# Performance work log

Hardware: AMD Instinct MI355X
Metric: run time of the kernel (lower is better)

Reference implementation:

```python
import jax, jax.numpy as jnp
import numpy as np
import math

B = 2; T = 512; ND = 256; NDAYS = 24; STRIDE = 4; KLEN = 14
DM = ND * KLEN          # 3584, d_model after unfolding
NLAYERS = 2; DSTATE = 16; DCONV = 4; EXPAND = 2
DI = EXPAND * DM        # 7168 d_inner
DTR = math.ceil(DM / 16)  # 224 dt_rank
NCLS = 41
LOUT = (T - KLEN) // STRIDE + 1  # 125


def setup_inputs():
    key = jax.random.key(0)
    ks = jax.random.split(key, 12)
    f32 = jnp.float32
    neuralInput = jax.random.normal(ks[0], (B, T, ND), f32)
    dayIdx = jax.random.randint(ks[1], (B,), 0, NDAYS)
    # day-specific linear init: identity weight, zero bias (as in BaseDecoder)
    day_w = jnp.tile(jnp.eye(ND, dtype=f32)[None], (NDAYS, 1, 1))
    day_b = jnp.zeros((NDAYS, 1, ND), f32)
    norm_w = jnp.ones((NLAYERS, DM), f32)
    norm_b = jnp.zeros((NLAYERS, DM), f32)
    in_proj_w = 0.02 * jax.random.normal(ks[2], (NLAYERS, 2 * DI, DM), f32)
    conv_w = 0.2 * jax.random.normal(ks[3], (NLAYERS, DI, DCONV), f32)  # depthwise
    conv_b = jnp.zeros((NLAYERS, DI), f32)
    x_proj_w = 0.02 * jax.random.normal(ks[4], (NLAYERS, DTR + 2 * DSTATE, DI), f32)
    s = DTR ** -0.5
    dt_proj_w = jax.random.uniform(ks[5], (NLAYERS, DI, DTR), f32, -s, s)
    # dt bias init: inverse-softplus of dt ~ LogUniform[1e-3, 1e-1]
    dt = jnp.exp(jax.random.uniform(ks[6], (NLAYERS, DI), f32) * (math.log(0.1) - math.log(0.001)) + math.log(0.001))
    dt = jnp.clip(dt, 1e-4, None)
    dt_proj_b = dt + jnp.log(-jnp.expm1(-dt))
    A_log = jnp.broadcast_to(jnp.log(jnp.arange(1, DSTATE + 1, dtype=f32)), (NLAYERS, DI, DSTATE)).copy()
    D_param = jnp.ones((NLAYERS, DI), f32)
    out_proj_w = 0.02 * jax.random.normal(ks[7], (NLAYERS, DM, DI), f32)
    normf_w = jnp.ones((DM,), f32)
    normf_b = jnp.zeros((DM,), f32)
    fc_w = 0.02 * jax.random.normal(ks[8], (NCLS, DM), f32)
    fc_b = jnp.zeros((NCLS,), f32)
    return dict(neuralInput=neuralInput, day_w=day_w, day_b=day_b, norm_w=norm_w, norm_b=norm_b,
                in_proj_w=in_proj_w, conv_w=conv_w, conv_b=conv_b, x_proj_w=x_proj_w,
                dt_proj_w=dt_proj_w, dt_proj_b=dt_proj_b, A_log=A_log, D_param=D_param,
                out_proj_w=out_proj_w, normf_w=normf_w, normf_b=normf_b, fc_w=fc_w, fc_b=fc_b,
                dayIdx=dayIdx)


def _layernorm(x, w, b):
    mu = x.mean(-1, keepdims=True)
    v = jnp.var(x, -1, keepdims=True)
    return (x - mu) * jax.lax.rsqrt(v + 1e-5) * w + b


def _mamba(h, ipw, cw, cb, xpw, dtw, dtb, Alog, Dp, opw):
    # h: (B, L, DM) -> (B, L, DM); unidirectional Mamba, use_fast_path=False math
    Bb, L, _ = h.shape
    xz = h @ ipw.T                              # (B, L, 2*DI)
    x, z = xz[..., :DI], xz[..., DI:]
    # depthwise causal conv1d, kernel DCONV, left pad DCONV-1, truncated to L
    xp = jnp.pad(x, ((0, 0), (DCONV - 1, 0), (0, 0)))
    xc = cb + sum(xp[:, j:j + L, :] * cw[:, j] for j in range(DCONV))
    x = jax.nn.silu(xc)
    x_dbl = x @ xpw.T                           # (B, L, DTR + 2*N)
    dt = x_dbl[..., :DTR]
    Bc = x_dbl[..., DTR:DTR + DSTATE]
    Cc = x_dbl[..., DTR + DSTATE:]
    delta = jax.nn.softplus(dt @ dtw.T + dtb)   # (B, L, DI), delta_softplus=True
    A = -jnp.exp(Alog)                          # (DI, N)
    dA = jnp.exp(delta[..., None] * A)          # (B, L, DI, N)
    dBu = (delta * x)[..., None] * Bc[:, :, None, :]  # (B, L, DI, N)

    def step(hst, inp):
        a, bu, c = inp
        hst = a * hst + bu                      # (B, DI, N)
        return hst, jnp.einsum('bdn,bn->bd', hst, c)

    h0 = jnp.zeros((Bb, DI, DSTATE), h.dtype)
    _, ys = jax.lax.scan(step, h0, (dA.transpose(1, 0, 2, 3), dBu.transpose(1, 0, 2, 3), Cc.transpose(1, 0, 2)))
    y = ys.transpose(1, 0, 2) + x * Dp          # skip term D*u
    y = y * jax.nn.silu(z)                      # gated output
    return y @ opw.T


def reference(neuralInput, day_w, day_b, norm_w, norm_b, in_proj_w, conv_w, conv_b, x_proj_w,
              dt_proj_w, dt_proj_b, A_log, D_param, out_proj_w, normf_w, normf_b, fc_w, fc_b, dayIdx):
    # --- BaseDecoder.forward_preprocessing (gaussianSmoothWidth = 0) ---
    t = jnp.einsum('btd,bdk->btk', neuralInput, day_w[dayIdx]) + day_b[dayIdx]
    t = t / (1.0 + jnp.abs(t))                  # Softsign
    idx = jnp.arange(LOUT)[:, None] * STRIDE + jnp.arange(KLEN)[None, :]
    win = t[:, idx, :]                          # (B, LOUT, KLEN, ND)
    # torch Unfold feature ordering: channel-major then kernel position -> d*KLEN + j
    h = win.transpose(0, 1, 3, 2).reshape(t.shape[0], LOUT, DM)
    # --- stacked Mamba blocks (pre-norm residual) ---
    residual = None
    for i in range(NLAYERS):
        residual = h if residual is None else h + residual
        hn = _layernorm(residual, norm_w[i], norm_b[i])
        h = _mamba(hn, in_proj_w[i], conv_w[i], conv_b[i], x_proj_w[i], dt_proj_w[i],
                   dt_proj_b[i], A_log[i], D_param[i], out_proj_w[i])
    residual = h + residual
    hn = _layernorm(residual, normf_w, normf_b)
    return hn @ fc_w.T + fc_b                   # (B, LOUT, NCLS)
```

## Files before the change

### kernel.cpp

```cpp
#include <hip/hip_runtime.h>
#include <hip/hip_bf16.h>
#include <math.h>

#define BATCH   2
#define TSEQ    512
#define NDIM    256
#define STRIDE_ 4
#define KLEN    14
#define DM      3584
#define DI      7168
#define DTR     224
#define DSTATE  16
#define NCLS    41
#define LOUT    125
#define LPAD    128
#define MROWS   256

typedef __attribute__((ext_vector_type(8))) short bf8_t;
typedef __attribute__((ext_vector_type(4))) float f4_t;

__device__ inline unsigned bfpair(float a, float b) {
    unsigned ua = __builtin_bit_cast(unsigned, a);
    unsigned ub = __builtin_bit_cast(unsigned, b);
    ua = (ua + 0x7fffu + ((ua >> 16) & 1u)) >> 16;
    ub = (ub + 0x7fffu + ((ub >> 16) & 1u)) >> 16;
    return ua | (ub << 16);
}
__device__ inline uint4 pack8(float4 a, float4 b) {
    return make_uint4(bfpair(a.x, a.y), bfpair(a.z, a.w),
                      bfpair(b.x, b.y), bfpair(b.z, b.w));
}

__global__ void day_proj(const float* __restrict__ nI, const float* __restrict__ dw,
                         const float* __restrict__ db, const int* __restrict__ dayIdx,
                         float* __restrict__ t_full) {
    int bi = blockIdx.x;
    int b = bi >> 9;
    int di = dayIdx[b];
    int tid = threadIdx.x;
    __shared__ float a_sh[256];
    a_sh[tid] = nI[(size_t)bi * 256 + tid];
    __syncthreads();
    const float* w = dw + (size_t)di * 65536;
    float acc = db[(size_t)di * 256 + tid];
    #pragma unroll 8
    for (int d = 0; d < 256; ++d) acc = fmaf(a_sh[d], w[d * 256 + tid], acc);
    t_full[(size_t)bi * 256 + tid] = acc / (1.f + fabsf(acc));
}

__global__ void window_k(const float* __restrict__ t_full, float* __restrict__ res) {
    int bl = blockIdx.x;
    int b = bl >> 7, l = bl & 127;
    size_t m = (size_t)b * LPAD + l;
    if (l >= LOUT) {
        for (int c = threadIdx.x; c < DM; c += 256) res[m * DM + c] = 0.f;
        return;
    }
    for (int c = threadIdx.x; c < DM; c += 256) {
        int d = c / KLEN, j = c - d * KLEN;
        res[m * DM + c] = t_full[((size_t)b * TSEQ + l * STRIDE_ + j) * 256 + d];
    }
}

__global__ void ln_pack(const float* __restrict__ res, const float* __restrict__ w,
                        const float* __restrict__ b, short* __restrict__ hnp) {
    int m = blockIdx.x, tid = threadIdx.x;
    const float* row = res + (size_t)m * DM;
    float s = 0.f, ss = 0.f;
    for (int c = tid; c < DM; c += 256) { float v = row[c]; s += v; ss += v * v; }
    #pragma unroll
    for (int o = 32; o; o >>= 1) { s += __shfl_xor(s, o); ss += __shfl_xor(ss, o); }
    __shared__ float sm[8];
    int wid = tid >> 6;
    if ((tid & 63) == 0) { sm[wid] = s; sm[4 + wid] = ss; }
    __syncthreads();
    s = sm[0] + sm[1] + sm[2] + sm[3];
    ss = sm[4] + sm[5] + sm[6] + sm[7];
    float mu = s * (1.f / DM);
    float var = ss * (1.f / DM) - mu * mu;
    float rs = rsqrtf(var + 1e-5f);
    for (int G = tid; G < DM / 8; G += 256) {
        float4 f0 = *(const float4*)(row + G * 8);
        float4 f1 = *(const float4*)(row + G * 8 + 4);
        float4 w0 = *(const float4*)(w + G * 8);
        float4 w1 = *(const float4*)(w + G * 8 + 4);
        float4 b0 = *(const float4*)(b + G * 8);
        float4 b1 = *(const float4*)(b + G * 8 + 4);
        f0.x = (f0.x - mu) * rs * w0.x + b0.x; f0.y = (f0.y - mu) * rs * w0.y + b0.y;
        f0.z = (f0.z - mu) * rs * w0.z + b0.z; f0.w = (f0.w - mu) * rs * w0.w + b0.w;
        f1.x = (f1.x - mu) * rs * w1.x + b1.x; f1.y = (f1.y - mu) * rs * w1.y + b1.y;
        f1.z = (f1.z - mu) * rs * w1.z + b1.z; f1.w = (f1.w - mu) * rs * w1.w + b1.w;
        *(uint4*)&hnp[((size_t)G * 256 + m) * 8] = pack8(f0, f1);
    }
}

__global__ void pack_rows(const float* __restrict__ src, int lda, int nG,
                          short* __restrict__ dst) {
    int m = blockIdx.x;
    const float* row = src + (size_t)m * lda;
    for (int G = threadIdx.x; G < nG; G += 256) {
        float4 f0 = *(const float4*)(row + G * 8);
        float4 f1 = *(const float4*)(row + G * 8 + 4);
        *(uint4*)&dst[((size_t)G * 256 + m) * 8] = pack8(f0, f1);
    }
}

__global__ void zero_k(float* __restrict__ p) {
    size_t i = (size_t)(blockIdx.x * 256 + threadIdx.x) * 4;
    *(float4*)(p + i) = make_float4(0.f, 0.f, 0.f, 0.f);
}

template <int EPI, int NT>
__global__ __launch_bounds__(256)
void gemm_mfma(const short* __restrict__ Ap, const float* __restrict__ W, int ldw,
               float* __restrict__ C, int ldc, int kSteps,
               const float* __restrict__ bias) {
    constexpr int NC = NT / 16;
    __shared__ __align__(16) short a_sh[2][4][2056];
    __shared__ __align__(16) short w_sh[2][4][NT * 8 + 8];
    const int tid = threadIdx.x;
    const int wz = tid >> 6, lane = tid & 63;
    const int g = lane >> 4, i16 = lane & 15;
    const int n0 = blockIdx.x * NT;
    const int sBeg = blockIdx.z * kSteps, sEnd = sBeg + kSteps;
    const int wr = tid >> 3;
    const int wq = tid & 7;

    f4_t acc[4][NC];
    #pragma unroll
    for (int r = 0; r < 4; ++r)
        #pragma unroll
        for (int c = 0; c < NC; ++c) acc[r][c] = (f4_t){0.f, 0.f, 0.f, 0.f};

    const short* arow = Ap + (size_t)tid * 8;
    const float* wbase  = W + (size_t)(n0 + wr) * ldw + wq * 4;
    const float* wbase2 = wbase + (size_t)32 * ldw;

    float4 wv0 = *(const float4*)(wbase + (size_t)sBeg * 32);
    float4 wv1;
    if constexpr (NT == 64) wv1 = *(const float4*)(wbase2 + (size_t)sBeg * 32);
    #pragma unroll
    for (int it = 0; it < 4; ++it)
        __builtin_amdgcn_global_load_lds(
            (const __attribute__((address_space(1))) unsigned int*)(arow + (size_t)(sBeg * 4 + it) * 2048),
            (__attribute__((address_space(3))) unsigned int*)&a_sh[0][it][tid * 8], 16, 0, 0);
    {
        uint2 p0 = {bfpair(wv0.x, wv0.y), bfpair(wv0.z, wv0.w)};
        *(uint2*)&w_sh[0][wq >> 1][wr * 8 + (wq & 1) * 4] = p0;
        if constexpr (NT == 64) {
            uint2 p1 = {bfpair(wv1.x, wv1.y), bfpair(wv1.z, wv1.w)};
            *(uint2*)&w_sh[0][wq >> 1][(wr + 32) * 8 + (wq & 1) * 4] = p1;
        }
    }
    int s1 = (sBeg + 1 < sEnd) ? sBeg + 1 : sEnd - 1;
    wv0 = *(const float4*)(wbase + (size_t)s1 * 32);
    if constexpr (NT == 64) wv1 = *(const float4*)(wbase2 + (size_t)s1 * 32);

    for (int s = sBeg; s < sEnd; ++s) {
        const int cur = (s - sBeg) & 1, nxt = cur ^ 1;
        __syncthreads();
        if (s + 1 < sEnd) {
            #pragma unroll
            for (int it = 0; it < 4; ++it)
                __builtin_amdgcn_global_load_lds(
                    (const __attribute__((address_space(1))) unsigned int*)(arow + (size_t)((s + 1) * 4 + it) * 2048),
                    (__attribute__((address_space(3))) unsigned int*)&a_sh[nxt][it][tid * 8], 16, 0, 0);
            uint2 p0 = {bfpair(wv0.x, wv0.y), bfpair(wv0.z, wv0.w)};
            *(uint2*)&w_sh[nxt][wq >> 1][wr * 8 + (wq & 1) * 4] = p0;
            if constexpr (NT == 64) {
                uint2 p1 = {bfpair(wv1.x, wv1.y), bfpair(wv1.z, wv1.w)};
                *(uint2*)&w_sh[nxt][wq >> 1][(wr + 32) * 8 + (wq & 1) * 4] = p1;
            }
            int s2 = (s + 2 < sEnd) ? s + 2 : sEnd - 1;
            wv0 = *(const float4*)(wbase + (size_t)s2 * 32);
            if constexpr (NT == 64) wv1 = *(const float4*)(wbase2 + (size_t)s2 * 32);
        }
        bf8_t af[4], wf[NC];
        #pragma unroll
        for (int r = 0; r < 4; ++r)
            af[r] = *(const bf8_t*)&a_sh[cur][g][(wz * 64 + r * 16 + i16) * 8];
        #pragma unroll
        for (int c = 0; c < NC; ++c)
            wf[c] = *(const bf8_t*)&w_sh[cur][g][(c * 16 + i16) * 8];
        #pragma unroll
        for (int r = 0; r < 4; ++r)
            #pragma unroll
            for (int c = 0; c < NC; ++c)
                acc[r][c] = __builtin_amdgcn_mfma_f32_16x16x32_bf16(af[r], wf[c], acc[r][c], 0, 0, 0);
    }

    float bv[NC];
    if (EPI == 1) {
        #pragma unroll
        for (int c = 0; c < NC; ++c) bv[c] = bias[n0 + c * 16 + i16];
    }
    #pragma unroll
    for (int r = 0; r < 4; ++r) {
        #pragma unroll
        for (int c = 0; c < NC; ++c) {
            int n = n0 + c * 16 + i16;
            #pragma unroll
            for (int v = 0; v < 4; ++v) {
                int m = wz * 64 + r * 16 + g * 4 + v;
                float val = acc[r][c][v];
                if (EPI == 0) {
                    C[(size_t)m * ldc + n] = val;
                } else if (EPI == 1) {
                    val += bv[c];
                    C[(size_t)m * ldc + n] = (val > 20.f) ? val : log1pf(expf(val));
                } else {
                    atomicAdd(&C[(size_t)m * ldc + n], val);
                }
            }
        }
    }
}

__global__ void conv_silu_pack(const float* __restrict__ xz, const float* __restrict__ cw,
                               const float* __restrict__ cb, float* __restrict__ xq,
                               short* __restrict__ xqp) {
    int bl = blockIdx.x;
    int b = bl / 125, l = bl % 125;
    size_t m = (size_t)b * LPAD + l;
    for (int c0 = threadIdx.x * 8; c0 < DI; c0 += 2048) {
        float v[8];
        float4 cb0 = *(const float4*)(cb + c0);
        float4 cb1 = *(const float4*)(cb + c0 + 4);
        v[0] = cb0.x; v[1] = cb0.y; v[2] = cb0.z; v[3] = cb0.w;
        v[4] = cb1.x; v[5] = cb1.y; v[6] = cb1.z; v[7] = cb1.w;
        #pragma unroll
        for (int j = 0; j < 4; ++j) {
            int lj = l - 3 + j;
            if (lj < 0) continue;
            const float* xr = xz + ((size_t)b * LPAD + lj) * (2 * DI) + c0;
            float4 x0 = *(const float4*)xr;
            float4 x1 = *(const float4*)(xr + 4);
            float xa[8] = {x0.x, x0.y, x0.z, x0.w, x1.x, x1.y, x1.z, x1.w};
            #pragma unroll
            for (int k = 0; k < 8; ++k)
                v[k] = fmaf(xa[k], cw[(c0 + k) * 4 + j], v[k]);
        }
        float4 o0, o1;
        #pragma unroll
        for (int k = 0; k < 8; ++k) {
            float sv = v[k] / (1.f + expf(-v[k]));
            if (k < 4) (&o0.x)[k] = sv; else (&o1.x)[k - 4] = sv;
        }
        *(float4*)(xq + m * DI + c0) = o0;
        *(float4*)(xq + m * DI + c0 + 4) = o1;
        *(uint4*)&xqp[(((size_t)c0 / 8) * 256 + m) * 8] = pack8(o0, o1);
    }
}

__global__ void scan_kernel(const float* __restrict__ delta, const float* __restrict__ xq,
                            const float* __restrict__ xdbl, const float* __restrict__ xz,
                            const float* __restrict__ Alog, const float* __restrict__ Dp,
                            float* __restrict__ y) {
    int tid = threadIdx.x;
    int sg = tid & 3;
    int c = blockIdx.x * 64 + (tid >> 2);
    int b = blockIdx.y;
    float As[4], st[4];
    #pragma unroll
    for (int k = 0; k < 4; ++k) {
        As[k] = -expf(Alog[(size_t)c * DSTATE + sg * 4 + k]);
        st[k] = 0.f;
    }
    float dp = Dp[c];
    size_t mb = (size_t)b * LPAD;
    float d_c = delta[mb * DI + c];
    float x_c = xq[mb * DI + c];
    float z_c = xz[mb * (2 * DI) + DI + c];
    float4 B_c = *(const float4*)(xdbl + mb * 256 + DTR + sg * 4);
    float4 C_c = *(const float4*)(xdbl + mb * 256 + DTR + DSTATE + sg * 4);
    for (int l = 0; l < LOUT; ++l) {
        float d_n = d_c, x_n = x_c, z_n = z_c;
        float4 B_n = B_c, C_n = C_c;
        if (l + 1 < LOUT) {
            size_t m = mb + l + 1;
            d_n = delta[m * DI + c];
            x_n = xq[m * DI + c];
            z_n = xz[m * (2 * DI) + DI + c];
            B_n = *(const float4*)(xdbl + m * 256 + DTR + sg * 4);
            C_n = *(const float4*)(xdbl + m * 256 + DTR + DSTATE + sg * 4);
        }
        float du = d_c * x_c;
        float yv = 0.f;
        #pragma unroll
        for (int k = 0; k < 4; ++k) {
            st[k] = fmaf(expf(d_c * As[k]), st[k], du * (&B_c.x)[k]);
            yv = fmaf(st[k], (&C_c.x)[k], yv);
        }
        yv += __shfl_xor(yv, 1);
        yv += __shfl_xor(yv, 2);
        if (sg == 0)
            y[(mb + l) * DI + c] = (yv + x_c * dp) * (z_c / (1.f + expf(-z_c)));
        d_c = d_n; x_c = x_n; z_c = z_n; B_c = B_n; C_c = C_n;
    }
}

__global__ void ln_fc(const float* __restrict__ res, const float* __restrict__ wf,
                      const float* __restrict__ bf, const float* __restrict__ fcw,
                      const float* __restrict__ fcb, float* __restrict__ out) {
    __shared__ __align__(16) float hs[DM];
    __shared__ float sm[8];
    int bl = blockIdx.x;
    int b = bl / 125, l = bl % 125;
    size_t m = (size_t)b * LPAD + l;
    int tid = threadIdx.x;
    const float* row = res + m * DM;
    float s = 0.f, ss = 0.f;
    for (int c = tid; c < DM; c += 256) { float v = row[c]; s += v; ss += v * v; }
    #pragma unroll
    for (int o = 32; o; o >>= 1) { s += __shfl_xor(s, o); ss += __shfl_xor(ss, o); }
    int wid = tid >> 6;
    if ((tid & 63) == 0) { sm[wid] = s; sm[4 + wid] = ss; }
    __syncthreads();
    s = sm[0] + sm[1] + sm[2] + sm[3];
    ss = sm[4] + sm[5] + sm[6] + sm[7];
    float mu = s * (1.f / DM);
    float var = ss * (1.f / DM) - mu * mu;
    float rs = rsqrtf(var + 1e-5f);
    for (int c = tid; c < DM; c += 256) hs[c] = (row[c] - mu) * rs * wf[c] + bf[c];
    __syncthreads();
    int lane = tid & 63;
    for (int n = wid; n < NCLS; n += 4) {
        const float* wrow = fcw + (size_t)n * DM;
        float a0 = 0.f, a1 = 0.f, a2 = 0.f, a3 = 0.f;
        for (int k = lane; k < DM; k += 256) {
            a0 = fmaf(hs[k],       wrow[k],       a0);
            a1 = fmaf(hs[k + 64],  wrow[k + 64],  a1);
            a2 = fmaf(hs[k + 128], wrow[k + 128], a2);
            a3 = fmaf(hs[k + 192], wrow[k + 192], a3);
        }
        float acc = (a0 + a1) + (a2 + a3);
        #pragma unroll
        for (int o = 32; o; o >>= 1) acc += __shfl_xor(acc, o);
        if (lane == 0) out[((size_t)b * LOUT + l) * NCLS + n] = acc + fcb[n];
    }
}

extern "C" void kernel_launch(void* const* d_in, const int* in_sizes, int n_in,
                              void* d_out, int out_size, void* d_ws, size_t ws_size,
                              hipStream_t stream) {
    (void)in_sizes; (void)n_in; (void)out_size; (void)ws_size;
    const float* nI   = (const float*)d_in[0];
    const float* dw   = (const float*)d_in[1];
    const float* db   = (const float*)d_in[2];
    const float* nw   = (const float*)d_in[3];
    const float* nb   = (const float*)d_in[4];
    const float* ipw  = (const float*)d_in[5];
    const float* cw   = (const float*)d_in[6];
    const float* cb   = (const float*)d_in[7];
    const float* xpw  = (const float*)d_in[8];
    const float* dtw  = (const float*)d_in[9];
    const float* dtb  = (const float*)d_in[10];
    const float* Alog = (const float*)d_in[11];
    const float* Dp   = (const float*)d_in[12];
    const float* opw  = (const float*)d_in[13];
    const float* nfw  = (const float*)d_in[14];
    const float* nfb  = (const float*)d_in[15];
    const float* fcw  = (const float*)d_in[16];
    const float* fcb  = (const float*)d_in[17];
    const int*   dayI = (const int*)d_in[18];
    float* out = (float*)d_out;

    float* wsf = (float*)d_ws;
    float* t_full = wsf; wsf += 262144;
    float* res    = wsf; wsf += (size_t)MROWS * DM;
    float* xz     = wsf; wsf += (size_t)MROWS * 2 * DI;
    float* xq     = wsf; wsf += (size_t)MROWS * DI;
    float* xdbl   = wsf; wsf += (size_t)MROWS * 256;
    float* delta  = wsf; wsf += (size_t)MROWS * DI;
    float* yb     = wsf; wsf += (size_t)MROWS * DI;
    short* wss = (short*)wsf;
    short* hnp   = wss; wss += (size_t)MROWS * DM;
    short* xqp   = wss; wss += (size_t)MROWS * DI;
    short* xdblp = wss; wss += (size_t)MROWS * DTR;
    short* ybp   = wss; wss += (size_t)MROWS * DI;

    day_proj<<<dim3(BATCH * TSEQ), 256, 0, stream>>>(nI, dw, db, dayI, t_full);
    window_k<<<dim3(MROWS), 256, 0, stream>>>(t_full, res);

    for (int i = 0; i < 2; ++i) {
        ln_pack<<<dim3(MROWS), 256, 0, stream>>>(res, nw + (size_t)i * DM, nb + (size_t)i * DM, hnp);
        gemm_mfma<0, 32><<<dim3(448, 1, 1), 256, 0, stream>>>(
            hnp, ipw + (size_t)i * 2 * DI * DM, DM, xz, 2 * DI, 112, nullptr);
        conv_silu_pack<<<dim3(BATCH * LOUT), 256, 0, stream>>>(
            xz, cw + (size_t)i * DI * 4, cb + (size_t)i * DI, xq, xqp);
        zero_k<<<dim3(64), 256, 0, stream>>>(xdbl);
        gemm_mfma<2, 32><<<dim3(8, 1, 28), 256, 0, stream>>>(
            xqp, xpw + (size_t)i * 256 * DI, DI, xdbl, 256, 8, nullptr);
        pack_rows<<<dim3(MROWS), 256, 0, stream>>>(xdbl, 256, DTR / 8, xdblp);
        gemm_mfma<1, 32><<<dim3(224, 1, 1), 256, 0, stream>>>(
            xdblp, dtw + (size_t)i * DI * DTR, DTR, delta, DI, 7, dtb + (size_t)i * DI);
        scan_kernel<<<dim3(DI / 64, BATCH), 256, 0, stream>>>(
            delta, xq, xdbl, xz, Alog + (size_t)i * DI * DSTATE, Dp + (size_t)i * DI, yb);
        pack_rows<<<dim3(MROWS), 256, 0, stream>>>(yb, DI, DI / 8, ybp);
        gemm_mfma<2, 32><<<dim3(112, 1, 4), 256, 0, stream>>>(
            ybp, opw + (size_t)i * DM * DI, DI, res, DM, 56, nullptr);
    }

    ln_fc<<<dim3(BATCH * LOUT), 256, 0, stream>>>(res, nfw, nfb, fcw, fcb, out);
}
```

Baseline: 1.381 ms.

## Triple-buffer GEMM loads and replace atomic split-K with partial buffers plus fused reduces

The bf16 MFMA GEMM moves from double to triple buffering in LDS. It uses explicit vmcnt waits and one barrier per k-step, so global-to-LDS copies run two steps ahead of compute. Split-K GEMMs no longer atomically add into a zeroed output. Each split instead writes its own partial slice, and the slices are summed in a new reduce_pack_bc kernel, inside ln_pack (residual add) and inside ln_fc. The zero and pack_rows kernels go away: the scan writes the packed bf16 y layout directly, and the reduce kernel packs xdbl. The cost is extra workspace and partial-sum traffic, plus scattered 2-byte stores from the scan.

```diff
diff --git a/kernel.cpp b/kernel.cpp
--- a/kernel.cpp
+++ b/kernel.cpp
@@ -62,15 +62,28 @@
     }
 }
 
-__global__ void ln_pack(const float* __restrict__ res, const float* __restrict__ w,
-                        const float* __restrict__ b, short* __restrict__ hnp) {
+template <bool ADD>
+__global__ void ln_pack(float* __restrict__ res, const float* __restrict__ part,
+                        const float* __restrict__ w, const float* __restrict__ b,
+                        short* __restrict__ hnp) {
+    __shared__ __align__(16) float hs[DM];
+    __shared__ float sm[8];
     int m = blockIdx.x, tid = threadIdx.x;
-    const float* row = res + (size_t)m * DM;
+    float* row = res + (size_t)m * DM;
     float s = 0.f, ss = 0.f;
-    for (int c = tid; c < DM; c += 256) { float v = row[c]; s += v; ss += v * v; }
+    for (int c = tid; c < DM; c += 256) {
+        float v = row[c];
+        if (ADD) {
+            v += part[((size_t)0 * MROWS + m) * DM + c]
+               + part[((size_t)1 * MROWS + m) * DM + c]
+               + part[((size_t)2 * MROWS + m) * DM + c]
+               + part[((size_t)3 * MROWS + m) * DM + c];
+            row[c] = v;
+        }
+        hs[c] = v; s += v; ss += v * v;
+    }
     #pragma unroll
     for (int o = 32; o; o >>= 1) { s += __shfl_xor(s, o); ss += __shfl_xor(ss, o); }
-    __shared__ float sm[8];
     int wid = tid >> 6;
     if ((tid & 63) == 0) { sm[wid] = s; sm[4 + wid] = ss; }
     __syncthreads();
@@ -80,8 +93,8 @@
     float var = ss * (1.f / DM) - mu * mu;
     float rs = rsqrtf(var + 1e-5f);
     for (int G = tid; G < DM / 8; G += 256) {
-        float4 f0 = *(const float4*)(row + G * 8);
-        float4 f1 = *(const float4*)(row + G * 8 + 4);
+        float4 f0 = *(const float4*)(hs + G * 8);
+        float4 f1 = *(const float4*)(hs + G * 8 + 4);
         float4 w0 = *(const float4*)(w + G * 8);
         float4 w1 = *(const float4*)(w + G * 8 + 4);
         float4 b0 = *(const float4*)(b + G * 8);
@@ -94,30 +107,14 @@
     }
 }
 
-__global__ void pack_rows(const float* __restrict__ src, int lda, int nG,
-                          short* __restrict__ dst) {
-    int m = blockIdx.x;
-    const float* row = src + (size_t)m * lda;
-    for (int G = threadIdx.x; G < nG; G += 256) {
-        float4 f0 = *(const float4*)(row + G * 8);
-        float4 f1 = *(const float4*)(row + G * 8 + 4);
-        *(uint4*)&dst[((size_t)G * 256 + m) * 8] = pack8(f0, f1);
-    }
-}
-
-__global__ void zero_k(float* __restrict__ p) {
-    size_t i = (size_t)(blockIdx.x * 256 + threadIdx.x) * 4;
-    *(float4*)(p + i) = make_float4(0.f, 0.f, 0.f, 0.f);
-}
-
 template <int EPI, int NT>
 __global__ __launch_bounds__(256)
 void gemm_mfma(const short* __restrict__ Ap, const float* __restrict__ W, int ldw,
-               float* __restrict__ C, int ldc, int kSteps,
+               float* __restrict__ C, int ldc, int kSteps, size_t cStrideZ,
                const float* __restrict__ bias) {
     constexpr int NC = NT / 16;
-    __shared__ __align__(16) short a_sh[2][4][2056];
-    __shared__ __align__(16) short w_sh[2][4][NT * 8 + 8];
+    __shared__ __align__(16) short a_sh[3][4][2056];
+    __shared__ __align__(16) short w_sh[3][4][NT * 8 + 8];
     const int tid = threadIdx.x;
     const int wz = tid >> 6, lane = tid & 63;
     const int g = lane >> 4, i16 = lane & 15;
@@ -125,6 +122,7 @@
     const int sBeg = blockIdx.z * kSteps, sEnd = sBeg + kSteps;
     const int wr = tid >> 3;
     const int wq = tid & 7;
+    C += (size_t)blockIdx.z * cStrideZ;
 
     f4_t acc[4][NC];
     #pragma unroll
@@ -133,47 +131,34 @@
         for (int c = 0; c < NC; ++c) acc[r][c] = (f4_t){0.f, 0.f, 0.f, 0.f};
 
     const short* arow = Ap + (size_t)tid * 8;
-    const float* wbase  = W + (size_t)(n0 + wr) * ldw + wq * 4;
-    const float* wbase2 = wbase + (size_t)32 * ldw;
-
+    const float* wbase = W + (size_t)(n0 + wr) * ldw + wq * 4;
+
+    auto stageA = [&](int s, int buf) {
+        #pragma unroll
+        for (int it = 0; it < 4; ++it)
+            __builtin_amdgcn_global_load_lds(
+                (const __attribute__((address_space(1))) unsigned int*)(arow + (size_t)(s * 4 + it) * 2048),
+                (__attribute__((address_space(3))) unsigned int*)&a_sh[buf][it][tid * 8], 16, 0, 0);
+    };
+
+    stageA(sBeg, 0);
     float4 wv0 = *(const float4*)(wbase + (size_t)sBeg * 32);
-    float4 wv1;
-    if constexpr (NT == 64) wv1 = *(const float4*)(wbase2 + (size_t)sBeg * 32);
-    #pragma unroll
-    for (int it = 0; it < 4; ++it)
-        __builtin_amdgcn_global_load_lds(
-            (const __attribute__((address_space(1))) unsigned int*)(arow + (size_t)(sBeg * 4 + it) * 2048),
-            (__attribute__((address_space(3))) unsigned int*)&a_sh[0][it][tid * 8], 16, 0, 0);
+    stageA(sBeg + 1, 1);
+    float4 wv1 = *(const float4*)(wbase + (size_t)(sBeg + 1) * 32);
     {
         uint2 p0 = {bfpair(wv0.x, wv0.y), bfpair(wv0.z, wv0.w)};
         *(uint2*)&w_sh[0][wq >> 1][wr * 8 + (wq & 1) * 4] = p0;
-        if constexpr (NT == 64) {
-            uint2 p1 = {bfpair(wv1.x, wv1.y), bfpair(wv1.z, wv1.w)};
-            *(uint2*)&w_sh[0][wq >> 1][(wr + 32) * 8 + (wq & 1) * 4] = p1;
-        }
-    }
-    int s1 = (sBeg + 1 < sEnd) ? sBeg + 1 : sEnd - 1;
-    wv0 = *(const float4*)(wbase + (size_t)s1 * 32);
-    if constexpr (NT == 64) wv1 = *(const float4*)(wbase2 + (size_t)s1 * 32);
-
-    for (int s = sBeg; s < sEnd; ++s) {
-        const int cur = (s - sBeg) & 1, nxt = cur ^ 1;
-        __syncthreads();
-        if (s + 1 < sEnd) {
-            #pragma unroll
-            for (int it = 0; it < 4; ++it)
-                __builtin_amdgcn_global_load_lds(
-                    (const __attribute__((address_space(1))) unsigned int*)(arow + (size_t)((s + 1) * 4 + it) * 2048),
-                    (__attribute__((address_space(3))) unsigned int*)&a_sh[nxt][it][tid * 8], 16, 0, 0);
-            uint2 p0 = {bfpair(wv0.x, wv0.y), bfpair(wv0.z, wv0.w)};
-            *(uint2*)&w_sh[nxt][wq >> 1][wr * 8 + (wq & 1) * 4] = p0;
-            if constexpr (NT == 64) {
-                uint2 p1 = {bfpair(wv1.x, wv1.y), bfpair(wv1.z, wv1.w)};
-                *(uint2*)&w_sh[nxt][wq >> 1][(wr + 32) * 8 + (wq & 1) * 4] = p1;
-            }
-            int s2 = (s + 2 < sEnd) ? s + 2 : sEnd - 1;
-            wv0 = *(const float4*)(wbase + (size_t)s2 * 32);
-            if constexpr (NT == 64) wv1 = *(const float4*)(wbase2 + (size_t)s2 * 32);
+    }
+    asm volatile("s_waitcnt vmcnt(5) lgkmcnt(0)" ::: "memory");
+    __builtin_amdgcn_s_barrier();
+
+    float4 wv2;
+    for (int t = sBeg; t < sEnd; ++t) {
+        const int cur = (t - sBeg) % 3;
+        const bool has2 = (t + 2 < sEnd);
+        if (has2) {
+            stageA(t + 2, (cur + 2) % 3);
+            wv2 = *(const float4*)(wbase + (size_t)(t + 2) * 32);
         }
         bf8_t af[4], wf[NC];
         #pragma unroll
@@ -187,6 +172,17 @@
             #pragma unroll
             for (int c = 0; c < NC; ++c)
                 acc[r][c] = __builtin_amdgcn_mfma_f32_16x16x32_bf16(af[r], wf[c], acc[r][c], 0, 0, 0);
+        if (t + 1 < sEnd) {
+            uint2 p1 = {bfpair(wv1.x, wv1.y), bfpair(wv1.z, wv1.w)};
+            *(uint2*)&w_sh[(cur + 1) % 3][wq >> 1][wr * 8 + (wq & 1) * 4] = p1;
+            if (has2) {
+                wv1 = wv2;
+                asm volatile("s_waitcnt vmcnt(5) lgkmcnt(0)" ::: "memory");
+            } else {
+                asm volatile("s_waitcnt vmcnt(0) lgkmcnt(0)" ::: "memory");
+            }
+            __builtin_amdgcn_s_barrier();
+        }
     }
 
     float bv[NC];
@@ -205,14 +201,29 @@
                 float val = acc[r][c][v];
                 if (EPI == 0) {
                     C[(size_t)m * ldc + n] = val;
-                } else if (EPI == 1) {
+                } else {
                     val += bv[c];
                     C[(size_t)m * ldc + n] = (val > 20.f) ? val : log1pf(expf(val));
-                } else {
-                    atomicAdd(&C[(size_t)m * ldc + n], val);
                 }
             }
         }
+    }
+}
+
+__global__ void reduce_pack_bc(const float* __restrict__ part, float* __restrict__ xdbl,
+                               short* __restrict__ xdblp) {
+    int m = blockIdx.x, tid = threadIdx.x;
+    float v = 0.f;
+    #pragma unroll 4
+    for (int z = 0; z < 28; ++z) v += part[((size_t)z * MROWS + m) * 256 + tid];
+    xdbl[(size_t)m * 256 + tid] = v;
+    __shared__ float buf[256];
+    buf[tid] = v;
+    __syncthreads();
+    if (tid < DTR / 8) {
+        float4 f0 = *(const float4*)&buf[tid * 8];
+        float4 f1 = *(const float4*)&buf[tid * 8 + 4];
+        *(uint4*)&xdblp[((size_t)tid * 256 + m) * 8] = pack8(f0, f1);
     }
 }
 
@@ -255,7 +266,7 @@
 __global__ void scan_kernel(const float* __restrict__ delta, const float* __restrict__ xq,
                             const float* __restrict__ xdbl, const float* __restrict__ xz,
                             const float* __restrict__ Alog, const float* __restrict__ Dp,
-                            float* __restrict__ y) {
+                            float* __restrict__ y, short* __restrict__ ybp) {
     int tid = threadIdx.x;
     int sg = tid & 3;
     int c = blockIdx.x * 64 + (tid >> 2);
@@ -293,15 +304,21 @@
         }
         yv += __shfl_xor(yv, 1);
         yv += __shfl_xor(yv, 2);
-        if (sg == 0)
-            y[(mb + l) * DI + c] = (yv + x_c * dp) * (z_c / (1.f + expf(-z_c)));
+        if (sg == 0) {
+            float yout = (yv + x_c * dp) * (z_c / (1.f + expf(-z_c)));
+            size_t m = mb + l;
+            y[m * DI + c] = yout;
+            ybp[((size_t)(c >> 3) * 256 + m) * 8 + (c & 7)] =
+                (short)(bfpair(yout, 0.f) & 0xffffu);
+        }
         d_c = d_n; x_c = x_n; z_c = z_n; B_c = B_n; C_c = C_n;
     }
 }
 
-__global__ void ln_fc(const float* __restrict__ res, const float* __restrict__ wf,
-                      const float* __restrict__ bf, const float* __restrict__ fcw,
-                      const float* __restrict__ fcb, float* __restrict__ out) {
+__global__ void ln_fc(const float* __restrict__ res, const float* __restrict__ part,
+                      const float* __restrict__ wf, const float* __restrict__ bf,
+                      const float* __restrict__ fcw, const float* __restrict__ fcb,
+                      float* __restrict__ out) {
     __shared__ __align__(16) float hs[DM];
     __shared__ float sm[8];
     int bl = blockIdx.x;
@@ -310,7 +327,14 @@
     int tid = threadIdx.x;
     const float* row = res + m * DM;
     float s = 0.f, ss = 0.f;
-    for (int c = tid; c < DM; c += 256) { float v = row[c]; s += v; ss += v * v; }
+    for (int c = tid; c < DM; c += 256) {
+        float v = row[c]
+                + part[((size_t)0 * MROWS + m) * DM + c]
+                + part[((size_t)1 * MROWS + m) * DM + c]
+                + part[((size_t)2 * MROWS + m) * DM + c]
+                + part[((size_t)3 * MROWS + m) * DM + c];
+        hs[c] = v; s += v; ss += v * v;
+    }
     #pragma unroll
     for (int o = 32; o; o >>= 1) { s += __shfl_xor(s, o); ss += __shfl_xor(ss, o); }
     int wid = tid >> 6;
@@ -321,7 +345,7 @@
     float mu = s * (1.f / DM);
     float var = ss * (1.f / DM) - mu * mu;
     float rs = rsqrtf(var + 1e-5f);
-    for (int c = tid; c < DM; c += 256) hs[c] = (row[c] - mu) * rs * wf[c] + bf[c];
+    for (int c = tid; c < DM; c += 256) hs[c] = (hs[c] - mu) * rs * wf[c] + bf[c];
     __syncthreads();
     int lane = tid & 63;
     for (int n = wid; n < NCLS; n += 4) {
@@ -366,13 +390,15 @@
     float* out = (float*)d_out;
 
     float* wsf = (float*)d_ws;
-    float* t_full = wsf; wsf += 262144;
-    float* res    = wsf; wsf += (size_t)MROWS * DM;
-    float* xz     = wsf; wsf += (size_t)MROWS * 2 * DI;
-    float* xq     = wsf; wsf += (size_t)MROWS * DI;
-    float* xdbl   = wsf; wsf += (size_t)MROWS * 256;
-    float* delta  = wsf; wsf += (size_t)MROWS * DI;
-    float* yb     = wsf; wsf += (size_t)MROWS * DI;
+    float* t_full   = wsf; wsf += 262144;
+    float* res      = wsf; wsf += (size_t)MROWS * DM;
+    float* xz       = wsf; wsf += (size_t)MROWS * 2 * DI;
+    float* xq       = wsf; wsf += (size_t)MROWS * DI;
+    float* xdbl     = wsf; wsf += (size_t)MROWS * 256;
+    float* delta    = wsf; wsf += (size_t)MROWS * DI;
+    float* yb       = wsf; wsf += (size_t)MROWS * DI;
+    float* xdbl_prt = wsf; wsf += (size_t)28 * MROWS * 256;
+    float* res_prt  = wsf; wsf += (size_t)4 * MROWS * DM;
     short* wss = (short*)wsf;
     short* hnp   = wss; wss += (size_t)MROWS * DM;
     short* xqp   = wss; wss += (size_t)MROWS * DI;
@@ -383,23 +409,28 @@
     window_k<<<dim3(MROWS), 256, 0, stream>>>(t_full, res);
 
     for (int i = 0; i < 2; ++i) {
-        ln_pack<<<dim3(MROWS), 256, 0, stream>>>(res, nw + (size_t)i * DM, nb + (size_t)i * DM, hnp);
+        if (i == 0)
+            ln_pack<false><<<dim3(MROWS), 256, 0, stream>>>(
+                res, nullptr, nw, nb, hnp);
+        else
+            ln_pack<true><<<dim3(MROWS), 256, 0, stream>>>(
+                res, res_prt, nw + (size_t)DM, nb + (size_t)DM, hnp);
         gemm_mfma<0, 32><<<dim3(448, 1, 1), 256, 0, stream>>>(
-            hnp, ipw + (size_t)i * 2 * DI * DM, DM, xz, 2 * DI, 112, nullptr);
+            hnp, ipw + (size_t)i * 2 * DI * DM, DM, xz, 2 * DI, 112, 0, nullptr);
         conv_silu_pack<<<dim3(BATCH * LOUT), 256, 0, stream>>>(
             xz, cw + (size_t)i * DI * 4, cb + (size_t)i * DI, xq, xqp);
-        zero_k<<<dim3(64), 256, 0, stream>>>(xdbl);
-        gemm_mfma<2, 32><<<dim3(8, 1, 28), 256, 0, stream>>>(
-            xqp, xpw + (size_t)i * 256 * DI, DI, xdbl, 256, 8, nullptr);
-        pack_rows<<<dim3(MROWS), 256, 0, stream>>>(xdbl, 256, DTR / 8, xdblp);
+        gemm_mfma<0, 32><<<dim3(8, 1, 28), 256, 0, stream>>>(
+            xqp, xpw + (size_t)i * 256 * DI, DI, xdbl_prt, 256, 8,
+            (size_t)MROWS * 256, nullptr);
+        reduce_pack_bc<<<dim3(MROWS), 256, 0, stream>>>(xdbl_prt, xdbl, xdblp);
         gemm_mfma<1, 32><<<dim3(224, 1, 1), 256, 0, stream>>>(
-            xdblp, dtw + (size_t)i * DI * DTR, DTR, delta, DI, 7, dtb + (size_t)i * DI);
+            xdblp, dtw + (size_t)i * DI * DTR, DTR, delta, DI, 7, 0, dtb + (size_t)i * DI);
         scan_kernel<<<dim3(DI / 64, BATCH), 256, 0, stream>>>(
-            delta, xq, xdbl, xz, Alog + (size_t)i * DI * DSTATE, Dp + (size_t)i * DI, yb);
-        pack_rows<<<dim3(MROWS), 256, 0, stream>>>(yb, DI, DI / 8, ybp);
-        gemm_mfma<2, 32><<<dim3(112, 1, 4), 256, 0, stream>>>(
-            ybp, opw + (size_t)i * DM * DI, DI, res, DM, 56, nullptr);
-    }
-
-    ln_fc<<<dim3(BATCH * LOUT), 256, 0, stream>>>(res, nfw, nfb, fcw, fcb, out);
-}
+            delta, xq, xdbl, xz, Alog + (size_t)i * DI * DSTATE, Dp + (size_t)i * DI, yb, ybp);
+        gemm_mfma<0, 32><<<dim3(112, 1, 4), 256, 0, stream>>>(
+            ybp, opw + (size_t)i * DM * DI, DI, res_prt, DM, 56,
+            (size_t)MROWS * DM, nullptr);
+    }
+
+    ln_fc<<<dim3(BATCH * LOUT), 256, 0, stream>>>(res, res_prt, nfw, nfb, fcw, fcb, out);
+}
```

After: 1.287 ms. 1.07x faster.
